# Optimization experiments

Measured on AMD Instinct MI355X. Metric: run time of the kernel, lower is better.

The kernel has to match this reference:

```python
import jax, jax.numpy as jnp
import numpy as np

BIAS_BASE = 1.0
HEADS = 8
TOPK = 32
NEG_INF = -1e30


def setup_inputs() -> dict:
    key = jax.random.key(0)
    ks = jax.random.split(key, 7)
    B, N, T, D = 8, 256, 128, 256
    s = 1.0 / np.sqrt(D)
    return {
        'h_val': jax.random.normal(ks[0], (B, N, T, D), jnp.float32),
        'z_map': jax.random.normal(ks[1], (B, N, D), jnp.float32),
        'base_adj': jax.random.uniform(ks[2], (B, N, N), jnp.float32),
        'Wq': jax.random.normal(ks[3], (D, D), jnp.float32) * s,
        'Wk': jax.random.normal(ks[4], (D, D), jnp.float32) * s,
        'Wv': jax.random.normal(ks[5], (D, D), jnp.float32) * s,
        'Wo': jax.random.normal(ks[6], (D, D), jnp.float32) * s,
    }


def reference(h_val, z_map, base_adj, Wq, Wk, Wv, Wo):
    B, N, T, D = h_val.shape
    H = HEADS
    hd = D // H
    scale = 1.0 / np.sqrt(hd)

    # q, k: [B, H, N, hd] (Linear with no bias: x @ W.T)
    q = (z_map @ Wq.T).reshape(B, N, H, hd).transpose(0, 2, 1, 3)
    k = (z_map @ Wk.T).reshape(B, N, H, hd).transpose(0, 2, 1, 3)

    scores = jnp.einsum('bhid,bhjd->bhij', q, k) * scale
    # log-adjacency bias, broadcast over heads
    bias = jnp.log(jnp.clip(base_adj, 1e-12, None))
    scores = scores + BIAS_BASE * bias[:, None, :, :]

    raw_attn = jax.nn.softmax(scores, axis=-1)

    # top-k mask: keep entries >= k-th largest per row (ties measure-zero for
    # continuous scores; matches torch.topk scatter mask)
    kth = jax.lax.top_k(scores, TOPK)[0][..., -1:]
    masked = jnp.where(scores >= kth, scores, NEG_INF)
    attn = jax.nn.softmax(masked, axis=-1)

    # v: [B, H, N, T, hd]
    v = (h_val @ Wv.T).reshape(B, N, T, H, hd).transpose(0, 3, 1, 2, 4)
    mixed = jnp.einsum('bhij,bhjtd->bhitd', attn, v)
    mixed = mixed.transpose(0, 2, 3, 1, 4).reshape(B, N, T, D)
    mixed = mixed @ Wo.T

    out = h_val + mixed  # dropout is identity in eval / p=0
    return out, attn.mean(axis=1), raw_attn.mean(axis=1)
```

## Files before the change

### kernel.cpp

```cpp
#include <hip/hip_runtime.h>
#include <stdint.h>

#define BB 8
#define NN 256
#define TT 128
#define DD 256
#define HH 8
#define HD 32
#define KTOP 32

typedef short bf16x8 __attribute__((ext_vector_type(8)));
typedef float f32x4 __attribute__((ext_vector_type(4)));

static __device__ __forceinline__ short f2bf(float f) {
  uint32_t u = __float_as_uint(f);
  u += 0x7FFFu + ((u >> 16) & 1u);
  return (short)(u >> 16);
}

static __device__ __forceinline__ uint32_t skey(float f) {
  uint32_t u = __float_as_uint(f);
  return (u & 0x80000000u) ? ~u : (u | 0x80000000u);
}

static __device__ __forceinline__ f32x4 mfma16(bf16x8 a, bf16x8 b, f32x4 c) {
  return __builtin_amdgcn_mfma_f32_16x16x32_bf16(a, b, c, 0, 0, 0);
}

__global__ __launch_bounds__(256) void k_cvt(const float* __restrict__ wv,
                                             const float* __restrict__ wo,
                                             short* __restrict__ wvb,
                                             short* __restrict__ wob) {
  int idx = blockIdx.x * 256 + threadIdx.x;
  wvb[idx] = f2bf(wv[idx]);
  wob[idx] = f2bf(wo[idx]);
}

__global__ __launch_bounds__(256) void k_qk(const float* __restrict__ z,
                                            const float* __restrict__ Wq,
                                            const float* __restrict__ Wk,
                                            float* __restrict__ q,
                                            float* __restrict__ kk) {
  int b = blockIdx.x >> 4;
  int i0 = (blockIdx.x & 15) * 16;
  __shared__ float zl[DD][16];
  int tid = threadIdx.x;
  for (int r = 0; r < 16; ++r)
    zl[tid][r] = z[(size_t)(b * NN + i0 + r) * DD + tid];
  __syncthreads();
  float aq[16], ak[16];
#pragma unroll
  for (int r = 0; r < 16; ++r) { aq[r] = 0.f; ak[r] = 0.f; }
  int o = tid;
  const float4* zc = reinterpret_cast<const float4*>(&zl[0][0]);
  for (int kx = 0; kx < DD; ++kx) {
    float wq = Wq[(size_t)o * DD + kx];
    float wk = Wk[(size_t)o * DD + kx];
    float zr[16];
    ((float4*)zr)[0] = zc[kx * 4 + 0];
    ((float4*)zr)[1] = zc[kx * 4 + 1];
    ((float4*)zr)[2] = zc[kx * 4 + 2];
    ((float4*)zr)[3] = zc[kx * 4 + 3];
#pragma unroll
    for (int r = 0; r < 16; ++r) {
      aq[r] = fmaf(zr[r], wq, aq[r]);
      ak[r] = fmaf(zr[r], wk, ak[r]);
    }
  }
  for (int r = 0; r < 16; ++r) {
    q[(size_t)(b * NN + i0 + r) * DD + o] = aq[r];
    kk[(size_t)(b * NN + i0 + r) * DD + o] = ak[r];
  }
}

__global__ __launch_bounds__(256) void k_attn(const float* __restrict__ q,
                                              const float* __restrict__ kmat,
                                              const float* __restrict__ adj,
                                              short* __restrict__ attn,
                                              float* __restrict__ attn_mean,
                                              float* __restrict__ raw_mean) {
  int b = blockIdx.x >> 8;
  int i = blockIdx.x & 255;
  __shared__ float ql[DD];
  __shared__ float bias[NN];
  __shared__ float sc[HH][NN];
  __shared__ float ms[HH], invraw[HH], invs2[HH];
  __shared__ uint32_t thr[HH];
  int tid = threadIdx.x;
  ql[tid] = q[(size_t)(b * NN + i) * DD + tid];
  bias[tid] = logf(fmaxf(adj[(size_t)(b * NN + i) * NN + tid], 1e-12f));
  __syncthreads();
  int wv = tid >> 6, lane = tid & 63;
  const float scale = 0.17677669529663687f;
  for (int hh = 0; hh < 2; ++hh) {
    int h = wv * 2 + hh;
    float sv[4];
#pragma unroll
    for (int c = 0; c < 4; ++c) {
      int j = lane + 64 * c;
      const float4* kp =
          (const float4*)&kmat[(size_t)(b * NN + j) * DD + h * HD];
      float s = 0.f;
#pragma unroll
      for (int d4 = 0; d4 < 8; ++d4) {
        float4 kv = kp[d4];
        s = fmaf(ql[h * HD + d4 * 4 + 0], kv.x, s);
        s = fmaf(ql[h * HD + d4 * 4 + 1], kv.y, s);
        s = fmaf(ql[h * HD + d4 * 4 + 2], kv.z, s);
        s = fmaf(ql[h * HD + d4 * 4 + 3], kv.w, s);
      }
      sv[c] = s * scale + bias[j];
      sc[h][j] = sv[c];
    }
    float m = fmaxf(fmaxf(sv[0], sv[1]), fmaxf(sv[2], sv[3]));
    for (int off = 32; off > 0; off >>= 1) m = fmaxf(m, __shfl_xor(m, off, 64));
    float e = expf(sv[0] - m) + expf(sv[1] - m) + expf(sv[2] - m) +
              expf(sv[3] - m);
    for (int off = 32; off > 0; off >>= 1) e += __shfl_xor(e, off, 64);
    uint32_t kb[4];
#pragma unroll
    for (int c = 0; c < 4; ++c) kb[c] = skey(sv[c]);
    uint32_t lo = 0u, hi = 0xFFFFFFFFu;
    for (int it = 0; it < 32; ++it) {
      uint32_t mid = (uint32_t)(((uint64_t)lo + (uint64_t)hi + 1ull) >> 1);
      int cnt = 0;
#pragma unroll
      for (int c = 0; c < 4; ++c)
        cnt += __popcll(__ballot(kb[c] >= mid));
      if (cnt >= KTOP) lo = mid; else hi = mid - 1u;
    }
    float e2 = 0.f;
#pragma unroll
    for (int c = 0; c < 4; ++c)
      e2 += (kb[c] >= lo) ? expf(sv[c] - m) : 0.f;
    for (int off = 32; off > 0; off >>= 1) e2 += __shfl_xor(e2, off, 64);
    if (lane == 0) {
      ms[h] = m; invraw[h] = 1.f / e; invs2[h] = 1.f / e2; thr[h] = lo;
    }
  }
  __syncthreads();
  int j = tid;
  float rm = 0.f, am = 0.f;
#pragma unroll
  for (int h = 0; h < HH; ++h) {
    float s = sc[h][j];
    float e = expf(s - ms[h]);
    rm += e * invraw[h];
    float a = (skey(s) >= thr[h]) ? e * invs2[h] : 0.f;
    am += a;
    attn[((size_t)(b * HH + h) * NN + i) * NN + j] = f2bf(a);
  }
  raw_mean[(size_t)(b * NN + i) * NN + j] = rm * 0.125f;
  attn_mean[(size_t)(b * NN + i) * NN + j] = am * 0.125f;
}

__global__ __launch_bounds__(256) void k_vproj(const float* __restrict__ hv,
                                               const short* __restrict__ wvb,
                                               short* __restrict__ vws) {
  int bid = blockIdx.x;
  int jb = bid & 3;
  int t = (bid >> 2) & (TT - 1);
  int b = bid >> 9;
  int j0 = jb * 64;
  __shared__ short wl[256 * 40];
  int tid = threadIdx.x, wv = tid >> 6, lane = tid & 63;
  int lrow = lane & 15, quad = lane >> 4;
  f32x4 acc[16];
#pragma unroll
  for (int m = 0; m < 16; ++m) acc[m] = (f32x4){0.f, 0.f, 0.f, 0.f};
  int j = j0 + wv * 16 + lrow;
  const float* hrow = &hv[((size_t)(b * NN + j) * TT + t) * DD];
  for (int kc = 0; kc < 8; ++kc) {
    __syncthreads();
    {
      const int4* src = (const int4*)&wvb[(size_t)tid * DD + kc * 32];
      int4* dst = (int4*)&wl[tid * 40];
      dst[0] = src[0]; dst[1] = src[1]; dst[2] = src[2]; dst[3] = src[3];
    }
    __syncthreads();
    const float4* hp = (const float4*)&hrow[kc * 32 + quad * 8];
    float4 f0 = hp[0], f1 = hp[1];
    bf16x8 bfrag;
    bfrag[0] = f2bf(f0.x); bfrag[1] = f2bf(f0.y);
    bfrag[2] = f2bf(f0.z); bfrag[3] = f2bf(f0.w);
    bfrag[4] = f2bf(f1.x); bfrag[5] = f2bf(f1.y);
    bfrag[6] = f2bf(f1.z); bfrag[7] = f2bf(f1.w);
#pragma unroll
    for (int mt = 0; mt < 16; ++mt) {
      const bf16x8* ap = (const bf16x8*)&wl[(mt * 16 + lrow) * 40 + quad * 8];
      acc[mt] = mfma16(*ap, bfrag, acc[mt]);
    }
  }
#pragma unroll
  for (int mt = 0; mt < 16; ++mt) {
#pragma unroll
    for (int r = 0; r < 4; ++r) {
      int o = mt * 16 + quad * 4 + r;
      int h = o >> 5, dp = o & 31;
      vws[(((size_t)(b * HH + h) * TT + t) * HD + dp) * NN + j] =
          f2bf(acc[mt][r]);
    }
  }
}

__global__ __launch_bounds__(256) void k_mix(const short* __restrict__ attn,
                                             const short* __restrict__ vws,
                                             short* __restrict__ mixed) {
  int bid = blockIdx.x;
  int ct = bid & 15;
  int it = (bid >> 4) & 1;
  int bh = bid >> 5;
  int b = bh >> 3, h = bh & 7;
  int i0 = it * 128, c0 = ct * 256;
  __shared__ short vl[256 * 40];
  int tid = threadIdx.x, wv = tid >> 6, lane = tid & 63;
  int lrow = lane & 15, quad = lane >> 4;
  f32x4 acc[2][16];
#pragma unroll
  for (int mi = 0; mi < 2; ++mi)
#pragma unroll
    for (int nt = 0; nt < 16; ++nt) acc[mi][nt] = (f32x4){0.f, 0.f, 0.f, 0.f};
  const short* abase = &attn[((size_t)bh * NN + i0) * NN];
  const short* vbase = &vws[(size_t)bh * 4096 * NN + (size_t)c0 * NN];
  for (int kc = 0; kc < 8; ++kc) {
    __syncthreads();
    {
      const int4* src = (const int4*)&vbase[(size_t)tid * NN + kc * 32];
      int4* dst = (int4*)&vl[tid * 40];
      dst[0] = src[0]; dst[1] = src[1]; dst[2] = src[2]; dst[3] = src[3];
    }
    __syncthreads();
    bf16x8 afrag[2];
#pragma unroll
    for (int mi = 0; mi < 2; ++mi)
      afrag[mi] = *(const bf16x8*)&abase[(size_t)((wv * 2 + mi) * 16 + lrow) *
                                             NN + kc * 32 + quad * 8];
#pragma unroll
    for (int nt = 0; nt < 16; ++nt) {
      bf16x8 bfrag = *(const bf16x8*)&vl[(nt * 16 + lrow) * 40 + quad * 8];
      acc[0][nt] = mfma16(afrag[0], bfrag, acc[0][nt]);
      acc[1][nt] = mfma16(afrag[1], bfrag, acc[1][nt]);
    }
  }
#pragma unroll
  for (int mi = 0; mi < 2; ++mi)
#pragma unroll
    for (int nt = 0; nt < 16; ++nt)
#pragma unroll
      for (int r = 0; r < 4; ++r) {
        int i = i0 + (wv * 2 + mi) * 16 + quad * 4 + r;
        int col = c0 + nt * 16 + lrow;
        int t = col >> 5, dp = col & 31;
        mixed[((size_t)(b * NN + i) * TT + t) * DD + h * HD + dp] =
            f2bf(acc[mi][nt][r]);
      }
}

__global__ __launch_bounds__(256) void k_out(const short* __restrict__ mixed,
                                             const short* __restrict__ wob,
                                             const float* __restrict__ hv,
                                             float* __restrict__ out) {
  size_t row0 = (size_t)blockIdx.x * 128;
  __shared__ short wl[256 * 40];
  int tid = threadIdx.x, wv = tid >> 6, lane = tid & 63;
  int lrow = lane & 15, quad = lane >> 4;
  f32x4 acc[2][16];
#pragma unroll
  for (int mi = 0; mi < 2; ++mi)
#pragma unroll
    for (int nt = 0; nt < 16; ++nt) acc[mi][nt] = (f32x4){0.f, 0.f, 0.f, 0.f};
  for (int kc = 0; kc < 8; ++kc) {
    __syncthreads();
    {
      const int4* src = (const int4*)&wob[(size_t)tid * DD + kc * 32];
      int4* dst = (int4*)&wl[tid * 40];
      dst[0] = src[0]; dst[1] = src[1]; dst[2] = src[2]; dst[3] = src[3];
    }
    __syncthreads();
    bf16x8 afrag[2];
#pragma unroll
    for (int mi = 0; mi < 2; ++mi)
      afrag[mi] = *(const bf16x8*)&mixed[(row0 + (wv * 2 + mi) * 16 + lrow) *
                                             DD + kc * 32 + quad * 8];
#pragma unroll
    for (int nt = 0; nt < 16; ++nt) {
      bf16x8 bfrag = *(const bf16x8*)&wl[(nt * 16 + lrow) * 40 + quad * 8];
      acc[0][nt] = mfma16(afrag[0], bfrag, acc[0][nt]);
      acc[1][nt] = mfma16(afrag[1], bfrag, acc[1][nt]);
    }
  }
#pragma unroll
  for (int mi = 0; mi < 2; ++mi)
#pragma unroll
    for (int nt = 0; nt < 16; ++nt)
#pragma unroll
      for (int r = 0; r < 4; ++r) {
        size_t row = row0 + (wv * 2 + mi) * 16 + quad * 4 + r;
        int o = nt * 16 + lrow;
        out[row * DD + o] = acc[mi][nt][r] + hv[row * DD + o];
      }
}

extern "C" void kernel_launch(void* const* d_in, const int* in_sizes, int n_in,
                              void* d_out, int out_size, void* d_ws,
                              size_t ws_size, hipStream_t stream) {
  (void)in_sizes; (void)n_in; (void)out_size; (void)ws_size;
  const float* hv  = (const float*)d_in[0];
  const float* z   = (const float*)d_in[1];
  const float* adj = (const float*)d_in[2];
  const float* Wq  = (const float*)d_in[3];
  const float* Wk  = (const float*)d_in[4];
  const float* Wv  = (const float*)d_in[5];
  const float* Wo  = (const float*)d_in[6];
  float* out = (float*)d_out;
  float* attn_mean = out + (size_t)BB * NN * TT * DD;
  float* raw_mean = attn_mean + (size_t)BB * NN * NN;

  char* ws = (char*)d_ws;
  float* q = (float*)ws;      ws += (size_t)BB * NN * DD * 4;
  float* k = (float*)ws;      ws += (size_t)BB * NN * DD * 4;
  short* wvb = (short*)ws;    ws += (size_t)DD * DD * 2;
  short* wob = (short*)ws;    ws += (size_t)DD * DD * 2;
  short* attn = (short*)ws;   ws += (size_t)BB * HH * NN * NN * 2;
  short* vws = (short*)ws;    ws += (size_t)BB * HH * TT * HD * NN * 2;
  short* mixed = (short*)ws;  ws += (size_t)BB * NN * TT * DD * 2;

  hipLaunchKernelGGL(k_cvt, dim3(DD * DD / 256), dim3(256), 0, stream,
                     Wv, Wo, wvb, wob);
  hipLaunchKernelGGL(k_qk, dim3(BB * 16), dim3(256), 0, stream,
                     z, Wq, Wk, q, k);
  hipLaunchKernelGGL(k_attn, dim3(BB * NN), dim3(256), 0, stream,
                     q, k, adj, attn, attn_mean, raw_mean);
  hipLaunchKernelGGL(k_vproj, dim3(BB * TT * 4), dim3(256), 0, stream,
                     hv, wvb, vws);
  hipLaunchKernelGGL(k_mix, dim3(BB * HH * 2 * 16), dim3(256), 0, stream,
                     attn, vws, mixed);
  hipLaunchKernelGGL(k_out, dim3((BB * NN * TT) / 128), dim3(256), 0, stream,
                     mixed, wob, hv, out);
}
```

Baseline: 972.3 us.

## Make output projection persistent with full Wo resident in LDS and prefetch

The output-projection kernel becomes persistent: 512 blocks of 512 threads each load the whole bf16 Wo matrix into padded shared memory once. Each wave then loops over 16-row tiles with a grid stride, prefetching the next tile's A fragments while it stores the current one. This removes the per-k-chunk Wo reload and the block barriers of the old 2048-block kernel. In exchange it uses about 135KB of LDS per block, which limits residency, and each wave now computes only one 16-row tile per iteration.

```diff
diff --git a/kernel.cpp b/kernel.cpp
--- a/kernel.cpp
+++ b/kernel.cpp
@@ -256,49 +256,64 @@
       }
 }
 
-__global__ __launch_bounds__(256) void k_out(const short* __restrict__ mixed,
-                                             const short* __restrict__ wob,
-                                             const float* __restrict__ hv,
-                                             float* __restrict__ out) {
-  size_t row0 = (size_t)blockIdx.x * 128;
-  __shared__ short wl[256 * 40];
-  int tid = threadIdx.x, wv = tid >> 6, lane = tid & 63;
+__global__ __launch_bounds__(512, 2) void k_out(const short* __restrict__ mixed,
+                                                const short* __restrict__ wob,
+                                                const float* __restrict__ hv,
+                                                float* __restrict__ out) {
+  __shared__ short wl[256 * 264];
+  int tid = threadIdx.x;
+  {
+    int row = tid >> 1, half = tid & 1;
+    const int4* src = (const int4*)&wob[(size_t)row * DD + half * 128];
+    int4* dst = (int4*)&wl[row * 264 + half * 128];
+#pragma unroll
+    for (int x = 0; x < 16; ++x) dst[x] = src[x];
+  }
+  __syncthreads();
+  int wv = tid >> 6, lane = tid & 63;
   int lrow = lane & 15, quad = lane >> 4;
-  f32x4 acc[2][16];
-#pragma unroll
-  for (int mi = 0; mi < 2; ++mi)
-#pragma unroll
-    for (int nt = 0; nt < 16; ++nt) acc[mi][nt] = (f32x4){0.f, 0.f, 0.f, 0.f};
-  for (int kc = 0; kc < 8; ++kc) {
-    __syncthreads();
-    {
-      const int4* src = (const int4*)&wob[(size_t)tid * DD + kc * 32];
-      int4* dst = (int4*)&wl[tid * 40];
-      dst[0] = src[0]; dst[1] = src[1]; dst[2] = src[2]; dst[3] = src[3];
-    }
-    __syncthreads();
-    bf16x8 afrag[2];
-#pragma unroll
-    for (int mi = 0; mi < 2; ++mi)
-      afrag[mi] = *(const bf16x8*)&mixed[(row0 + (wv * 2 + mi) * 16 + lrow) *
-                                             DD + kc * 32 + quad * 8];
+  int gw = blockIdx.x * 8 + wv;
+  bf16x8 afrag[8];
+  {
+    const short* arow = &mixed[((size_t)gw * 16 + lrow) * DD];
+#pragma unroll
+    for (int kc = 0; kc < 8; ++kc)
+      afrag[kc] = *(const bf16x8*)&arow[kc * 32 + quad * 8];
+  }
+  for (int mt = gw; mt < 16384; mt += 4096) {
+    f32x4 acc[16];
+#pragma unroll
+    for (int nt = 0; nt < 16; ++nt) acc[nt] = (f32x4){0.f, 0.f, 0.f, 0.f};
+#pragma unroll
+    for (int kc = 0; kc < 8; ++kc) {
+#pragma unroll
+      for (int nt = 0; nt < 16; ++nt) {
+        bf16x8 bfrag =
+            *(const bf16x8*)&wl[(nt * 16 + lrow) * 264 + kc * 32 + quad * 8];
+        acc[nt] = mfma16(afrag[kc], bfrag, acc[nt]);
+      }
+    }
+    int mt2 = mt + 4096;
+    bf16x8 anext[8];
+    if (mt2 < 16384) {
+      const short* arow = &mixed[((size_t)mt2 * 16 + lrow) * DD];
+#pragma unroll
+      for (int kc = 0; kc < 8; ++kc)
+        anext[kc] = *(const bf16x8*)&arow[kc * 32 + quad * 8];
+    }
+    size_t row0 = (size_t)mt * 16;
 #pragma unroll
     for (int nt = 0; nt < 16; ++nt) {
-      bf16x8 bfrag = *(const bf16x8*)&wl[(nt * 16 + lrow) * 40 + quad * 8];
-      acc[0][nt] = mfma16(afrag[0], bfrag, acc[0][nt]);
-      acc[1][nt] = mfma16(afrag[1], bfrag, acc[1][nt]);
-    }
-  }
-#pragma unroll
-  for (int mi = 0; mi < 2; ++mi)
-#pragma unroll
-    for (int nt = 0; nt < 16; ++nt)
 #pragma unroll
       for (int r = 0; r < 4; ++r) {
-        size_t row = row0 + (wv * 2 + mi) * 16 + quad * 4 + r;
+        size_t row = row0 + quad * 4 + r;
         int o = nt * 16 + lrow;
-        out[row * DD + o] = acc[mi][nt][r] + hv[row * DD + o];
+        out[row * DD + o] = acc[nt][r] + hv[row * DD + o];
       }
+    }
+#pragma unroll
+    for (int kc = 0; kc < 8; ++kc) afrag[kc] = anext[kc];
+  }
 }
 
 extern "C" void kernel_launch(void* const* d_in, const int* in_sizes, int n_in,
@@ -335,6 +350,6 @@
                      hv, wvb, vws);
   hipLaunchKernelGGL(k_mix, dim3(BB * HH * 2 * 16), dim3(256), 0, stream,
                      attn, vws, mixed);
-  hipLaunchKernelGGL(k_out, dim3((BB * NN * TT) / 128), dim3(256), 0, stream,
+  hipLaunchKernelGGL(k_out, dim3(512), dim3(512), 0, stream,
                      mixed, wob, hv, out);
 }
```

New measurement: 1.565 ms. 1.61x slower.

## Split output projection by column halves with full-K swizzled Wo tile in LDS

Applied to the files above, without the earlier changes.

k_out now splits the 256 output columns across two blocks, doubling the grid. Each block loads its full 128x256 Wo slice into LDS once, using an XOR swizzle to avoid bank conflicts, and preloads all A fragments into registers, so the per-k-chunk syncthreads loop goes away. The accumulator count per thread is halved, and launch bounds are set to allow two blocks per CU. The trade-off is 64KB of LDS per block and each mixed row being read by two blocks.

```diff
diff --git a/kernel.cpp b/kernel.cpp
--- a/kernel.cpp
+++ b/kernel.cpp
@@ -256,49 +256,69 @@
       }
 }
 
-__global__ __launch_bounds__(256) void k_out(const short* __restrict__ mixed,
-                                             const short* __restrict__ wob,
-                                             const float* __restrict__ hv,
-                                             float* __restrict__ out) {
-  size_t row0 = (size_t)blockIdx.x * 128;
-  __shared__ short wl[256 * 40];
-  int tid = threadIdx.x, wv = tid >> 6, lane = tid & 63;
+__global__ __launch_bounds__(256, 2) void k_out(const short* __restrict__ mixed,
+                                                const short* __restrict__ wob,
+                                                const float* __restrict__ hv,
+                                                float* __restrict__ out) {
+  __shared__ short wl[128 * 256];
+  int tid = threadIdx.x;
+  int half = blockIdx.x & 1;
+  size_t row0 = (size_t)(blockIdx.x >> 1) * 128;
+  int wv = tid >> 6, lane = tid & 63;
   int lrow = lane & 15, quad = lane >> 4;
-  f32x4 acc[2][16];
+
+  bf16x8 afrag[2][8];
+  {
+    const short* a0 = &mixed[(row0 + wv * 32 + lrow) * DD];
+    const short* a1 = &mixed[(row0 + wv * 32 + 16 + lrow) * DD];
+#pragma unroll
+    for (int kc = 0; kc < 8; ++kc) {
+      afrag[0][kc] = *(const bf16x8*)&a0[kc * 32 + quad * 8];
+      afrag[1][kc] = *(const bf16x8*)&a1[kc * 32 + quad * 8];
+    }
+  }
+  {
+    int row = tid >> 1, seg = tid & 1;
+    const int4* src =
+        (const int4*)&wob[(size_t)(half * 128 + row) * DD + seg * 128];
+#pragma unroll
+    for (int g = 0; g < 16; ++g) {
+      int gg = seg * 16 + g;
+      int dstb = row * 512 + ((gg * 16) ^ ((row & 7) << 4));
+      *(int4*)((char*)wl + dstb) = src[g];
+    }
+  }
+  __syncthreads();
+
+  f32x4 acc[2][8];
 #pragma unroll
   for (int mi = 0; mi < 2; ++mi)
 #pragma unroll
-    for (int nt = 0; nt < 16; ++nt) acc[mi][nt] = (f32x4){0.f, 0.f, 0.f, 0.f};
+    for (int nt = 0; nt < 8; ++nt) acc[mi][nt] = (f32x4){0.f, 0.f, 0.f, 0.f};
+#pragma unroll
   for (int kc = 0; kc < 8; ++kc) {
-    __syncthreads();
-    {
-      const int4* src = (const int4*)&wob[(size_t)tid * DD + kc * 32];
-      int4* dst = (int4*)&wl[tid * 40];
-      dst[0] = src[0]; dst[1] = src[1]; dst[2] = src[2]; dst[3] = src[3];
-    }
-    __syncthreads();
-    bf16x8 afrag[2];
-#pragma unroll
-    for (int mi = 0; mi < 2; ++mi)
-      afrag[mi] = *(const bf16x8*)&mixed[(row0 + (wv * 2 + mi) * 16 + lrow) *
-                                             DD + kc * 32 + quad * 8];
-#pragma unroll
-    for (int nt = 0; nt < 16; ++nt) {
-      bf16x8 bfrag = *(const bf16x8*)&wl[(nt * 16 + lrow) * 40 + quad * 8];
-      acc[0][nt] = mfma16(afrag[0], bfrag, acc[0][nt]);
-      acc[1][nt] = mfma16(afrag[1], bfrag, acc[1][nt]);
-    }
-  }
+#pragma unroll
+    for (int nt = 0; nt < 8; ++nt) {
+      int brow = nt * 16 + lrow;
+      int boff = brow * 512 + ((kc * 64 + quad * 16) ^ ((brow & 7) << 4));
+      bf16x8 bfrag = *(const bf16x8*)((const char*)wl + boff);
+      acc[0][nt] = mfma16(afrag[0][kc], bfrag, acc[0][nt]);
+      acc[1][nt] = mfma16(afrag[1][kc], bfrag, acc[1][nt]);
+    }
+  }
+  __syncthreads();
+
 #pragma unroll
   for (int mi = 0; mi < 2; ++mi)
 #pragma unroll
-    for (int nt = 0; nt < 16; ++nt)
-#pragma unroll
-      for (int r = 0; r < 4; ++r) {
-        size_t row = row0 + (wv * 2 + mi) * 16 + quad * 4 + r;
-        int o = nt * 16 + lrow;
+    for (int r = 0; r < 4; ++r) {
+      size_t row = row0 + wv * 32 + mi * 16 + quad * 4 + r;
+#pragma unroll
+      for (int nt = 0; nt < 8; ++nt) {
+        int o = half * 128 + nt * 16 + lrow;
         out[row * DD + o] = acc[mi][nt][r] + hv[row * DD + o];
       }
+    }
 }
 
 extern "C" void kernel_launch(void* const* d_in, const int* in_sizes, int n_in,
@@ -335,6 +355,6 @@
                      hv, wvb, vws);
   hipLaunchKernelGGL(k_mix, dim3(BB * HH * 2 * 16), dim3(256), 0, stream,
                      attn, vws, mixed);
-  hipLaunchKernelGGL(k_out, dim3((BB * NN * TT) / 128), dim3(256), 0, stream,
-                     mixed, wob, hv, out);
-}
+  hipLaunchKernelGGL(k_out, dim3((BB * NN * TT / 128) * 2), dim3(256), 0,
+                     stream, mixed, wob, hv, out);
+}
```

Measured after the change: 931.5 us. 1.04x faster.
